# Performance work log

Hardware: AMD Instinct MI355X
Metric: run time of the kernel (lower is better)

The kernel has to match this reference:

```python
import jax, jax.numpy as jnp
import numpy as np

B, C_IN, C_INT, C_OUT, H, W = 4, 1024, 256, 1024, 64, 64
EPS = 1e-5

def conv1x1(x, w, b):
    # x: (B, Cin, H, W), w: (Cout, Cin), b: (Cout,)
    return jnp.einsum('bchw,oc->bohw', x, w) + b[None, :, None, None]

def batchnorm_eval(x, gamma, beta, mean, var):
    inv = gamma / jnp.sqrt(var + EPS)
    return x * inv[None, :, None, None] + (beta - mean * inv)[None, :, None, None]

def setup_inputs() -> dict:
    key = jax.random.key(0)
    ks = jax.random.split(key, 8)
    s_in = 1.0 / np.sqrt(C_IN)
    s_int = 1.0 / np.sqrt(C_INT)
    return {
        'x': jax.random.normal(ks[0], (B, C_IN, H, W), dtype=jnp.float32),
        'w_key': jax.random.normal(ks[1], (C_INT, C_IN), dtype=jnp.float32) * s_in,
        'b_key': jnp.zeros((C_INT,), dtype=jnp.float32),
        'gamma': jnp.ones((C_INT,), dtype=jnp.float32),
        'beta': jnp.zeros((C_INT,), dtype=jnp.float32),
        'mean': jnp.zeros((C_INT,), dtype=jnp.float32),
        'var': jnp.ones((C_INT,), dtype=jnp.float32),
        'w_value': jax.random.normal(ks[2], (C_INT, C_IN), dtype=jnp.float32) * s_in,
        'b_value': jax.random.normal(ks[3], (C_INT,), dtype=jnp.float32) * 0.1,
        'w_out': jax.random.normal(ks[4], (C_OUT, C_INT), dtype=jnp.float32) * s_int,
        'b_out': jax.random.normal(ks[5], (C_OUT,), dtype=jnp.float32) * 0.1,
    }

def reference(x, w_key, b_key, gamma, beta, mean, var, w_value, b_value, w_out, b_out):
    Bb, _, h, w = x.shape
    N = h * w
    # value: 1x1 conv, (B, C, N) -> (B, N, C)
    value = conv1x1(x, w_value, b_value).reshape(Bb, C_INT, N).transpose(0, 2, 1)
    # query/key share the same conv+BN (f_query = f_key)
    qk = batchnorm_eval(conv1x1(x, w_key, b_key), gamma, beta, mean, var).reshape(Bb, C_INT, N)
    query = qk.transpose(0, 2, 1)  # (B, N, C)
    key = qk                        # (B, C, N)
    sim = jnp.einsum('bnc,bcm->bnm', query, key) * (C_INT ** -0.5)  # (B, N, N)
    sim = jax.nn.softmax(sim, axis=-1)
    context = jnp.einsum('bnm,bmc->bnc', sim, value)  # (B, N, C)
    context = context.transpose(0, 2, 1).reshape(Bb, C_INT, h, w)
    return conv1x1(context, w_out, b_out)
```

## Files before the change

kernel.cpp:

```cpp
#include <hip/hip_runtime.h>

#define BATCH 4
#define CIN   1024
#define CI    256
#define CO    1024
#define NSP   4096

typedef __attribute__((ext_vector_type(8))) short bf16x8;
typedef __attribute__((ext_vector_type(4))) float f32x4;
typedef __attribute__((ext_vector_type(2))) unsigned uint2v;

struct __align__(8) us4 { unsigned short x, y, z, w; };

#define DEVI __device__ __forceinline__

DEVI unsigned short f2bf(float f) {
  union { float f; unsigned u; } un; un.f = f;
  unsigned u = un.u;
  u += 0x7FFFu + ((u >> 16) & 1u);
  return (unsigned short)(u >> 16);
}

DEVI unsigned cvtpk(float lo, float hi) {
  unsigned r;
  asm("v_cvt_pk_bf16_f32 %0, %1, %2" : "=v"(r) : "v"(lo), "v"(hi));
  return r;
}

DEVI void gl2lds16(const void* g, void* l) {
  __builtin_amdgcn_global_load_lds(
      (const __attribute__((address_space(1))) void*)g,
      (__attribute__((address_space(3))) void*)l, 16, 0, 0);
}

DEVI f32x4 mfma16(bf16x8 a, bf16x8 b, f32x4 c) {
  return __builtin_amdgcn_mfma_f32_16x16x32_bf16(a, b, c, 0, 0, 0);
}

__global__ __launch_bounds__(256) void k_prep(
    const float* __restrict__ w_key, const float* __restrict__ w_val,
    const float* __restrict__ w_out,
    const float* __restrict__ gamma, const float* __restrict__ beta,
    const float* __restrict__ mean,  const float* __restrict__ var,
    const float* __restrict__ b_key,
    unsigned short* __restrict__ wkv, unsigned short* __restrict__ wob,
    float* __restrict__ sq, float* __restrict__ bq)
{
  int idx = blockIdx.x * 256 + threadIdx.x;
  float wv = (idx < 262144) ? w_key[idx] : w_val[idx - 262144];
  wkv[idx] = f2bf(wv);
  if (idx < 262144) wob[idx] = f2bf(w_out[idx]);
  if (idx < 256) {
    float inv = gamma[idx] * rsqrtf(var[idx] + 1e-5f);
    sq[idx] = 0.25f * inv;
    bq[idx] = 0.25f * (beta[idx] + (b_key[idx] - mean[idx]) * inv);
  }
}

__global__ __launch_bounds__(256) void k_xpose(const float* __restrict__ x,
                                               unsigned short* __restrict__ xT)
{
  __shared__ unsigned short tile[64][65];
  int b = blockIdx.z, k0 = blockIdx.y * 64, n0 = blockIdx.x * 64;
  int tid = threadIdx.x;
  int rr = tid >> 4, cc = tid & 15;
  const float* xb = x + ((size_t)b * CIN + k0) * NSP + n0;
#pragma unroll
  for (int p = 0; p < 4; ++p) {
    int row = p * 16 + rr;
    float4 v = *(const float4*)(xb + (size_t)row * NSP + cc * 4);
    tile[row][cc * 4 + 0] = f2bf(v.x);
    tile[row][cc * 4 + 1] = f2bf(v.y);
    tile[row][cc * 4 + 2] = f2bf(v.z);
    tile[row][cc * 4 + 3] = f2bf(v.w);
  }
  __syncthreads();
  unsigned short* xtb = xT + ((size_t)b * NSP + n0) * CIN + k0;
#pragma unroll
  for (int p = 0; p < 4; ++p) {
    int n = p * 16 + rr;
    int kq = cc * 4;
    us4 pk;
    pk.x = tile[kq + 0][n]; pk.y = tile[kq + 1][n];
    pk.z = tile[kq + 2][n]; pk.w = tile[kq + 3][n];
    *(us4*)(xtb + (size_t)n * CIN + kq) = pk;
  }
}

template<int KDIM>
DEVI void gemm_core(const unsigned short* __restrict__ Ab,
                    const unsigned short* __restrict__ Bb,
                    unsigned short* ldsA, unsigned short* ldsB,
                    f32x4 acc[4][4], int tid)
{
  const int lane = tid & 63, wave = tid >> 6;
  const int q = lane >> 4, ln = lane & 15;
  const int wm = wave & 1, wn = wave >> 1;

  int aoff[4][2], boff[4][2];
#pragma unroll
  for (int f = 0; f < 4; ++f) {
    int ra = wm * 64 + f * 16 + ln;
    aoff[f][0] = (ra * 8 + ((q)     ^ (ra & 7))) * 8;
    aoff[f][1] = (ra * 8 + ((q + 4) ^ (ra & 7))) * 8;
    int rb = wn * 64 + f * 16 + ln;
    boff[f][0] = (rb * 8 + ((q)     ^ (rb & 7))) * 8;
    boff[f][1] = (rb * 8 + ((q + 4) ^ (rb & 7))) * 8;
  }
  int sgo[4];
#pragma unroll
  for (int i = 0; i < 4; ++i) {
    int s = i * 256 + tid;
    int row = s >> 3;
    int c8 = (s & 7) ^ (row & 7);
    sgo[i] = row * KDIM + c8 * 8;
  }
  for (int k0 = 0; k0 < KDIM; k0 += 64) {
#pragma unroll
    for (int i = 0; i < 4; ++i) {
      gl2lds16(Ab + sgo[i] + k0, ldsA + (i * 256 + wave * 64) * 8);
      gl2lds16(Bb + sgo[i] + k0, ldsB + (i * 256 + wave * 64) * 8);
    }
    __syncthreads();
#pragma unroll
    for (int kk = 0; kk < 2; ++kk) {
      bf16x8 af[4], bfr[4];
#pragma unroll
      for (int f = 0; f < 4; ++f) af[f]  = *(const bf16x8*)(ldsA + aoff[f][kk]);
#pragma unroll
      for (int f = 0; f < 4; ++f) bfr[f] = *(const bf16x8*)(ldsB + boff[f][kk]);
#pragma unroll
      for (int mf = 0; mf < 4; ++mf)
#pragma unroll
        for (int nf = 0; nf < 4; ++nf)
          acc[mf][nf] = mfma16(af[mf], bfr[nf], acc[mf][nf]);
    }
    __syncthreads();
  }
}

__global__ __launch_bounds__(256) void k_convqkv(
    const unsigned short* __restrict__ wkv,
    const unsigned short* __restrict__ xT,
    const float* __restrict__ sq, const float* __restrict__ bq,
    const float* __restrict__ bval,
    unsigned short* __restrict__ qkT,
    unsigned short* __restrict__ vv)
{
  __shared__ __align__(16) unsigned short ldsA[128 * 64];
  __shared__ __align__(16) unsigned short ldsB[128 * 64];
  int b = blockIdx.z, m0 = blockIdx.y * 128, n0 = blockIdx.x * 128;
  int tid = threadIdx.x;
  f32x4 z = {0.f, 0.f, 0.f, 0.f};
  f32x4 acc[4][4];
#pragma unroll
  for (int i = 0; i < 4; ++i)
#pragma unroll
    for (int j = 0; j < 4; ++j) acc[i][j] = z;

  gemm_core<CIN>(wkv + (size_t)m0 * CIN, xT + ((size_t)b * NSP + n0) * CIN,
                 ldsA, ldsB, acc, tid);

  int lane = tid & 63, wave = tid >> 6, q = lane >> 4, ln = lane & 15;
  int wm = wave & 1, wn = wave >> 1;
  if (m0 < 256) {
#pragma unroll
    for (int mf = 0; mf < 4; ++mf) {
      int cb = m0 + wm * 64 + mf * 16 + q * 4;
      float s0_ = sq[cb + 0], s1_ = sq[cb + 1], s2_ = sq[cb + 2], s3_ = sq[cb + 3];
      float b0_ = bq[cb + 0], b1_ = bq[cb + 1], b2_ = bq[cb + 2], b3_ = bq[cb + 3];
#pragma unroll
      for (int nf = 0; nf < 4; ++nf) {
        int n = n0 + wn * 64 + nf * 16 + ln;
        us4 pk;
        pk.x = f2bf(acc[mf][nf][0] * s0_ + b0_);
        pk.y = f2bf(acc[mf][nf][1] * s1_ + b1_);
        pk.z = f2bf(acc[mf][nf][2] * s2_ + b2_);
        pk.w = f2bf(acc[mf][nf][3] * s3_ + b3_);
        *(us4*)(qkT + ((size_t)b * NSP + n) * CI + cb) = pk;
      }
    }
  } else {
#pragma unroll
    for (int mf = 0; mf < 4; ++mf) {
      int cb = (m0 - 256) + wm * 64 + mf * 16 + q * 4;
#pragma unroll
      for (int r = 0; r < 4; ++r) {
        float bv = bval[cb + r];
#pragma unroll
        for (int nf = 0; nf < 4; ++nf) {
          int n = n0 + wn * 64 + nf * 16 + ln;
          vv[((size_t)b * CI + (cb + r)) * NSP + n] = f2bf(acc[mf][nf][r] + bv);
        }
      }
    }
  }
}

__global__ __launch_bounds__(256, 2) void k_attn_part(
    const unsigned short* __restrict__ qkT,
    const unsigned short* __restrict__ vv,
    float* __restrict__ Opart,
    float* __restrict__ Lpart)
{
  __shared__ __align__(16) unsigned short Kt[2][32 * 256];
  __shared__ __align__(16) unsigned short Vt[2][256 * 32];
  __shared__ __align__(16) unsigned short Pl[4 * 32 * 40];

  int bid = blockIdx.x;
  int slice = bid & 15, qt = bid >> 4;
  int b = slice >> 2, js = slice & 3;
  int n0 = qt * 128;
  int tid = threadIdx.x, lane = tid & 63, wave = tid >> 6;
  int q = lane >> 4, ln = lane & 15;
  const unsigned short* qkb = qkT + (size_t)b * NSP * CI;
  const unsigned short* vb  = vv  + (size_t)b * CI * NSP;

  bf16x8 Qf0[8], Qf1[8];
  {
    const unsigned short* qr0 = qkb + (size_t)(n0 + wave * 32 + ln) * CI + q * 8;
    const unsigned short* qr1 = qr0 + 16 * CI;
#pragma unroll
    for (int t = 0; t < 8; ++t) Qf0[t] = *(const bf16x8*)(qr0 + t * 32);
#pragma unroll
    for (int t = 0; t < 8; ++t) Qf1[t] = *(const bf16x8*)(qr1 + t * 32);
  }

  int kbA = (ln * 32 + ((q ^ (ln & 7)) & 7)) * 8;
  int kbB = (ln * 32 + (((4 + q) ^ (ln & 7)) & 7)) * 8;
  int vbase = (ln * 4 + ((q ^ ((ln >> 1) & 3)) & 3)) * 8;

  unsigned short* Plw = Pl + wave * (32 * 40);
  int pw0 = ln * 40 + q * 4;
  int pw1 = ln * 40 + 16 + q * 4;
  int pw2 = (ln + 16) * 40 + q * 4;
  int pw3 = (ln + 16) * 40 + 16 + q * 4;
  int pr0 = ln * 40 + q * 8;
  int pr1 = (ln + 16) * 40 + q * 8;

  int gko[4], gvo[4];
#pragma unroll
  for (int i = 0; i < 4; ++i) {
    int s = i * 256 + tid;
    int j = s >> 5, f = s & 31;
    gko[i] = j * CI + ((f & 24) | ((f ^ j) & 7)) * 8;
    int c = s >> 2;
    gvo[i] = c * NSP + ((s ^ (c >> 1)) & 3) * 8;
  }

  f32x4 O0[16], O1[16];
  f32x4 z = {0.f, 0.f, 0.f, 0.f};
#pragma unroll
  for (int cf = 0; cf < 16; ++cf) { O0[cf] = z; O1[cf] = z; }
  float l0c = 0.f, l1c = 0.f;

  int jbase = js * 1024;

#pragma unroll
  for (int i = 0; i < 4; ++i)
    gl2lds16(qkb + (size_t)jbase * CI + gko[i], &Kt[0][(i * 256 + wave * 64) * 8]);
#pragma unroll
  for (int i = 0; i < 4; ++i)
    gl2lds16(vb + jbase + gvo[i], &Vt[0][(i * 256 + wave * 64) * 8]);
  __syncthreads();

  for (int it = 0; it < 32; ++it) {
    int cur = it & 1;

    if (it < 31) {
      int j1 = jbase + (it + 1) * 32;
#pragma unroll
      for (int i = 0; i < 4; ++i)
        gl2lds16(qkb + (size_t)j1 * CI + gko[i],
                 &Kt[cur ^ 1][(i * 256 + wave * 64) * 8]);
#pragma unroll
      for (int i = 0; i < 4; ++i)
        gl2lds16(vb + j1 + gvo[i],
                 &Vt[cur ^ 1][(i * 256 + wave * 64) * 8]);
    }

    const unsigned short* Kc = Kt[cur];
    const unsigned short* Vc = Vt[cur];

    f32x4 s0 = z, s1 = z, s2 = z, s3 = z;
    __builtin_amdgcn_s_setprio(1);
#pragma unroll
    for (int t = 0; t < 8; ++t) {
      int ko = ((t & 1) ? kbB : kbA) + (t >> 1) * 64;
      bf16x8 kf0 = *(const bf16x8*)(Kc + ko);
      bf16x8 kf1 = *(const bf16x8*)(Kc + ko + 4096);
      s0 = mfma16(kf0, Qf0[t], s0);
      s1 = mfma16(kf1, Qf0[t], s1);
      s2 = mfma16(kf0, Qf1[t], s2);
      s3 = mfma16(kf1, Qf1[t], s3);
    }
    __builtin_amdgcn_s_setprio(0);

    float p00 = __expf(s0[0]), p01 = __expf(s0[1]);
    float p02 = __expf(s0[2]), p03 = __expf(s0[3]);
    float p04 = __expf(s1[0]), p05 = __expf(s1[1]);
    float p06 = __expf(s1[2]), p07 = __expf(s1[3]);
    float p10 = __expf(s2[0]), p11 = __expf(s2[1]);
    float p12 = __expf(s2[2]), p13 = __expf(s2[3]);
    float p14 = __expf(s3[0]), p15 = __expf(s3[1]);
    float p16 = __expf(s3[2]), p17 = __expf(s3[3]);

    uint2v w;
    w.x = cvtpk(p00, p01); w.y = cvtpk(p02, p03);
    *(uint2v*)(Plw + pw0) = w;
    w.x = cvtpk(p04, p05); w.y = cvtpk(p06, p07);
    *(uint2v*)(Plw + pw1) = w;
    w.x = cvtpk(p10, p11); w.y = cvtpk(p12, p13);
    *(uint2v*)(Plw + pw2) = w;
    w.x = cvtpk(p14, p15); w.y = cvtpk(p16, p17);
    *(uint2v*)(Plw + pw3) = w;

    l0c += ((p00 + p01) + (p02 + p03)) + ((p04 + p05) + (p06 + p07));
    l1c += ((p10 + p11) + (p12 + p13)) + ((p14 + p15) + (p16 + p17));

    bf16x8 pf0 = *(const bf16x8*)(Plw + pr0);
    bf16x8 pf1 = *(const bf16x8*)(Plw + pr1);
    __builtin_amdgcn_s_setprio(1);
#pragma unroll
    for (int cf = 0; cf < 16; ++cf) {
      bf16x8 vf = *(const bf16x8*)(Vc + vbase + cf * 512);
      O0[cf] = mfma16(pf0, vf, O0[cf]);
      O1[cf] = mfma16(pf1, vf, O1[cf]);
    }
    __builtin_amdgcn_s_setprio(0);

    __syncthreads();
  }

  l0c += __shfl_xor(l0c, 16); l0c += __shfl_xor(l0c, 32);
  l1c += __shfl_xor(l1c, 16); l1c += __shfl_xor(l1c, 32);

  float* Ob = Opart + (size_t)bid * (128 * 256);
  if (lane < 16) {
    Lpart[bid * 128 + wave * 32 + lane] = l0c;
    Lpart[bid * 128 + wave * 32 + 16 + lane] = l1c;
  }
#pragma unroll
  for (int r = 0; r < 4; ++r) {
    int r0 = wave * 32 + q * 4 + r;
#pragma unroll
    for (int cf = 0; cf < 16; ++cf) {
      Ob[r0 * 256 + cf * 16 + ln] = O0[cf][r];
      Ob[(r0 + 16) * 256 + cf * 16 + ln] = O1[cf][r];
    }
  }
}

__global__ __launch_bounds__(256) void k_merge(
    const float* __restrict__ Opart,
    const float* __restrict__ Lpart,
    unsigned short* __restrict__ ctx)
{
  __shared__ float Winv[64];
  int mb = blockIdx.x;
  int b = mb >> 6, qg = mb & 63;
  int qt = qg >> 1, half = qg & 1;
  int ro = half * 64;
  int tid = threadIdx.x;
  int pb0 = qt * 16 + b * 4;

  if (tid < 64) {
    float L = Lpart[(pb0 + 0) * 128 + ro + tid]
            + Lpart[(pb0 + 1) * 128 + ro + tid]
            + Lpart[(pb0 + 2) * 128 + ro + tid]
            + Lpart[(pb0 + 3) * 128 + ro + tid];
    Winv[tid] = 1.0f / L;
  }
  __syncthreads();

  const float* O0 = Opart + ((size_t)(pb0 + 0) * 128 + ro) * 256;
  const float* O1 = Opart + ((size_t)(pb0 + 1) * 128 + ro) * 256;
  const float* O2 = Opart + ((size_t)(pb0 + 2) * 128 + ro) * 256;
  const float* O3 = Opart + ((size_t)(pb0 + 3) * 128 + ro) * 256;
  unsigned short* cb = ctx + ((size_t)b * NSP + qg * 64) * CI;
#pragma unroll 4
  for (int row = 0; row < 64; ++row) {
    float a = (O0[row * 256 + tid] + O1[row * 256 + tid]
             + O2[row * 256 + tid] + O3[row * 256 + tid]) * Winv[row];
    cb[(size_t)row * CI + tid] = f2bf(a);
  }
}

__global__ __launch_bounds__(256) void k_convout(
    const unsigned short* __restrict__ wo,
    const unsigned short* __restrict__ ctx,
    const float* __restrict__ bout,
    float* __restrict__ out)
{
  __shared__ __align__(16) unsigned short ldsA[128 * 64];
  __shared__ __align__(16) unsigned short ldsB[128 * 64];
  int b = blockIdx.z, m0 = blockIdx.y * 128, n0 = blockIdx.x * 128;
  int tid = threadIdx.x;
  f32x4 z = {0.f, 0.f, 0.f, 0.f};
  f32x4 acc[4][4];
#pragma unroll
  for (int i = 0; i < 4; ++i)
#pragma unroll
    for (int j = 0; j < 4; ++j) acc[i][j] = z;

  gemm_core<CI>(wo + (size_t)m0 * CI, ctx + ((size_t)b * NSP + n0) * CI,
                ldsA, ldsB, acc, tid);

  int lane = tid & 63, wave = tid >> 6, q = lane >> 4, ln = lane & 15;
  int wm = wave & 1, wn = wave >> 1;
#pragma unroll
  for (int mf = 0; mf < 4; ++mf) {
    int cb = m0 + wm * 64 + mf * 16 + q * 4;
    float bo0 = bout[cb + 0], bo1 = bout[cb + 1], bo2 = bout[cb + 2], bo3 = bout[cb + 3];
#pragma unroll
    for (int nf = 0; nf < 4; ++nf) {
      int n = n0 + wn * 64 + nf * 16 + ln;
      float* p = out + ((size_t)b * CO + cb) * NSP + n;
      p[0 * (size_t)NSP] = acc[mf][nf][0] + bo0;
      p[1 * (size_t)NSP] = acc[mf][nf][1] + bo1;
      p[2 * (size_t)NSP] = acc[mf][nf][2] + bo2;
      p[3 * (size_t)NSP] = acc[mf][nf][3] + bo3;
    }
  }
}

extern "C" void kernel_launch(void* const* d_in, const int* in_sizes, int n_in,
                              void* d_out, int out_size, void* d_ws, size_t ws_size,
                              hipStream_t stream) {
  const float* x     = (const float*)d_in[0];
  const float* w_key = (const float*)d_in[1];
  const float* b_key = (const float*)d_in[2];
  const float* gamma = (const float*)d_in[3];
  const float* beta  = (const float*)d_in[4];
  const float* mean  = (const float*)d_in[5];
  const float* var   = (const float*)d_in[6];
  const float* w_val = (const float*)d_in[7];
  const float* b_val = (const float*)d_in[8];
  const float* w_out = (const float*)d_in[9];
  const float* b_out = (const float*)d_in[10];
  float* out = (float*)d_out;

  char* ws = (char*)d_ws;
  unsigned short* xT  = (unsigned short*)(ws);
  unsigned short* wkv = (unsigned short*)(ws + 33554432);
  unsigned short* wob = (unsigned short*)(ws + 34603008);
  unsigned short* qkT = (unsigned short*)(ws + 35127296);
  unsigned short* vv  = (unsigned short*)(ws + 43515904);
  unsigned short* ctx = (unsigned short*)(ws + 51904512);
  float* sq = (float*)(ws + 60293120);
  float* bq = (float*)(ws + 60294144);
  float* Opart = (float*)(ws + 60295168);
  float* Lpart = (float*)(ws + 127404032);

  k_prep<<<2048, 256, 0, stream>>>(w_key, w_val, w_out, gamma, beta, mean, var,
                                   b_key, wkv, wob, sq, bq);
  k_xpose<<<dim3(64, 16, 4), 256, 0, stream>>>(x, xT);
  k_convqkv<<<dim3(32, 4, 4), 256, 0, stream>>>(wkv, xT, sq, bq, b_val, qkT, vv);
  k_attn_part<<<512, 256, 0, stream>>>(qkT, vv, Opart, Lpart);
  k_merge<<<256, 256, 0, stream>>>(Opart, Lpart, ctx);
  k_convout<<<dim3(32, 8, 4), 256, 0, stream>>>(wob, ctx, b_out, out);
}
```

Measured before the change: 274.8 us.

## Store attention partials in bf16, double-buffer QKV GEMM, pack transpose writes

The split-attention partial outputs are now packed as bf16 pairs instead of fp32, which halves the Opart write and read traffic between the attention and merge kernels. The merge kernel is rewritten to unpack these pairs and map rows to match. The QKV conv GEMM gets a double-buffered LDS pipeline that prefetches the next K tile while the current one is being computed. The transpose kernel now writes packed 32-bit bf16 pairs with a padded tile. Storing unnormalized partials in bf16 costs some accuracy, and double-buffering doubles LDS use in the conv kernel.

```diff
diff --git a/kernel.cpp b/kernel.cpp
--- a/kernel.cpp
+++ b/kernel.cpp
@@ -60,7 +60,7 @@
 __global__ __launch_bounds__(256) void k_xpose(const float* __restrict__ x,
                                                unsigned short* __restrict__ xT)
 {
-  __shared__ unsigned short tile[64][65];
+  __shared__ unsigned short tile[64][66];
   int b = blockIdx.z, k0 = blockIdx.y * 64, n0 = blockIdx.x * 64;
   int tid = threadIdx.x;
   int rr = tid >> 4, cc = tid & 15;
@@ -69,10 +69,8 @@
   for (int p = 0; p < 4; ++p) {
     int row = p * 16 + rr;
     float4 v = *(const float4*)(xb + (size_t)row * NSP + cc * 4);
-    tile[row][cc * 4 + 0] = f2bf(v.x);
-    tile[row][cc * 4 + 1] = f2bf(v.y);
-    tile[row][cc * 4 + 2] = f2bf(v.z);
-    tile[row][cc * 4 + 3] = f2bf(v.w);
+    *(unsigned*)&tile[row][cc * 4 + 0] = cvtpk(v.x, v.y);
+    *(unsigned*)&tile[row][cc * 4 + 2] = cvtpk(v.z, v.w);
   }
   __syncthreads();
   unsigned short* xtb = xT + ((size_t)b * NSP + n0) * CIN + k0;
@@ -139,6 +137,71 @@
   }
 }
 
+template<int KDIM>
+DEVI void gemm_core_db(const unsigned short* __restrict__ Ab,
+                       const unsigned short* __restrict__ Bb,
+                       unsigned short* ldsA, unsigned short* ldsB,
+                       f32x4 acc[4][4], int tid)
+{
+  const int lane = tid & 63, wave = tid >> 6;
+  const int q = lane >> 4, ln = lane & 15;
+  const int wm = wave & 1, wn = wave >> 1;
+
+  int aoff[4][2], boff[4][2];
+#pragma unroll
+  for (int f = 0; f < 4; ++f) {
+    int ra = wm * 64 + f * 16 + ln;
+    aoff[f][0] = (ra * 8 + ((q)     ^ (ra & 7))) * 8;
+    aoff[f][1] = (ra * 8 + ((q + 4) ^ (ra & 7))) * 8;
+    int rb = wn * 64 + f * 16 + ln;
+    boff[f][0] = (rb * 8 + ((q)     ^ (rb & 7))) * 8;
+    boff[f][1] = (rb * 8 + ((q + 4) ^ (rb & 7))) * 8;
+  }
+  int sgo[4];
+#pragma unroll
+  for (int i = 0; i < 4; ++i) {
+    int s = i * 256 + tid;
+    int row = s >> 3;
+    int c8 = (s & 7) ^ (row & 7);
+    sgo[i] = row * KDIM + c8 * 8;
+  }
+#pragma unroll
+  for (int i = 0; i < 4; ++i) {
+    gl2lds16(Ab + sgo[i], ldsA + (i * 256 + wave * 64) * 8);
+    gl2lds16(Bb + sgo[i], ldsB + (i * 256 + wave * 64) * 8);
+  }
+  __syncthreads();
+
+  for (int k0 = 0; k0 < KDIM; k0 += 64) {
+    const int cur = (k0 >> 6) & 1;
+    unsigned short* A = ldsA + cur * (128 * 64);
+    unsigned short* B = ldsB + cur * (128 * 64);
+    if (k0 + 64 < KDIM) {
+      unsigned short* An = ldsA + (cur ^ 1) * (128 * 64);
+      unsigned short* Bn = ldsB + (cur ^ 1) * (128 * 64);
+#pragma unroll
+      for (int i = 0; i < 4; ++i) {
+        gl2lds16(Ab + sgo[i] + k0 + 64, An + (i * 256 + wave * 64) * 8);
+        gl2lds16(Bb + sgo[i] + k0 + 64, Bn + (i * 256 + wave * 64) * 8);
+      }
+    }
+#pragma unroll
+    for (int kk = 0; kk < 2; ++kk) {
+      bf16x8 af[4], bfr[4];
+#pragma unroll
+      for (int f = 0; f < 4; ++f) af[f]  = *(const bf16x8*)(A + aoff[f][kk]);
+#pragma unroll
+      for (int f = 0; f < 4; ++f) bfr[f] = *(const bf16x8*)(B + boff[f][kk]);
+#pragma unroll
+      for (int mf = 0; mf < 4; ++mf)
+#pragma unroll
+        for (int nf = 0; nf < 4; ++nf)
+          acc[mf][nf] = mfma16(af[mf], bfr[nf], acc[mf][nf]);
+    }
+    __syncthreads();
+  }
+}
+
 __global__ __launch_bounds__(256) void k_convqkv(
     const unsigned short* __restrict__ wkv,
     const unsigned short* __restrict__ xT,
@@ -147,8 +210,8 @@
     unsigned short* __restrict__ qkT,
     unsigned short* __restrict__ vv)
 {
-  __shared__ __align__(16) unsigned short ldsA[128 * 64];
-  __shared__ __align__(16) unsigned short ldsB[128 * 64];
+  __shared__ __align__(16) unsigned short ldsA[2 * 128 * 64];
+  __shared__ __align__(16) unsigned short ldsB[2 * 128 * 64];
   int b = blockIdx.z, m0 = blockIdx.y * 128, n0 = blockIdx.x * 128;
   int tid = threadIdx.x;
   f32x4 z = {0.f, 0.f, 0.f, 0.f};
@@ -158,8 +221,8 @@
 #pragma unroll
     for (int j = 0; j < 4; ++j) acc[i][j] = z;
 
-  gemm_core<CIN>(wkv + (size_t)m0 * CIN, xT + ((size_t)b * NSP + n0) * CIN,
-                 ldsA, ldsB, acc, tid);
+  gemm_core_db<CIN>(wkv + (size_t)m0 * CIN, xT + ((size_t)b * NSP + n0) * CIN,
+                    ldsA, ldsB, acc, tid);
 
   int lane = tid & 63, wave = tid >> 6, q = lane >> 4, ln = lane & 15;
   int wm = wave & 1, wn = wave >> 1;
@@ -200,7 +263,7 @@
 __global__ __launch_bounds__(256, 2) void k_attn_part(
     const unsigned short* __restrict__ qkT,
     const unsigned short* __restrict__ vv,
-    float* __restrict__ Opart,
+    unsigned* __restrict__ Opart,
     float* __restrict__ Lpart)
 {
   __shared__ __align__(16) unsigned short Kt[2][32 * 256];
@@ -335,24 +398,22 @@
   l0c += __shfl_xor(l0c, 16); l0c += __shfl_xor(l0c, 32);
   l1c += __shfl_xor(l1c, 16); l1c += __shfl_xor(l1c, 32);
 
-  float* Ob = Opart + (size_t)bid * (128 * 256);
+  unsigned* Ob = Opart + (size_t)bid * (64 * 256);
   if (lane < 16) {
     Lpart[bid * 128 + wave * 32 + lane] = l0c;
     Lpart[bid * 128 + wave * 32 + 16 + lane] = l1c;
   }
 #pragma unroll
   for (int r = 0; r < 4; ++r) {
-    int r0 = wave * 32 + q * 4 + r;
-#pragma unroll
-    for (int cf = 0; cf < 16; ++cf) {
-      Ob[r0 * 256 + cf * 16 + ln] = O0[cf][r];
-      Ob[(r0 + 16) * 256 + cf * 16 + ln] = O1[cf][r];
-    }
+    int rp = wave * 16 + q * 4 + r;
+#pragma unroll
+    for (int cf = 0; cf < 16; ++cf)
+      Ob[rp * 256 + cf * 16 + ln] = cvtpk(O0[cf][r], O1[cf][r]);
   }
 }
 
 __global__ __launch_bounds__(256) void k_merge(
-    const float* __restrict__ Opart,
+    const unsigned* __restrict__ Opart,
     const float* __restrict__ Lpart,
     unsigned short* __restrict__ ctx)
 {
@@ -360,29 +421,36 @@
   int mb = blockIdx.x;
   int b = mb >> 6, qg = mb & 63;
   int qt = qg >> 1, half = qg & 1;
-  int ro = half * 64;
   int tid = threadIdx.x;
   int pb0 = qt * 16 + b * 4;
 
   if (tid < 64) {
-    float L = Lpart[(pb0 + 0) * 128 + ro + tid]
-            + Lpart[(pb0 + 1) * 128 + ro + tid]
-            + Lpart[(pb0 + 2) * 128 + ro + tid]
-            + Lpart[(pb0 + 3) * 128 + ro + tid];
+    int row = half * 64 + tid;
+    float L = Lpart[(pb0 + 0) * 128 + row]
+            + Lpart[(pb0 + 1) * 128 + row]
+            + Lpart[(pb0 + 2) * 128 + row]
+            + Lpart[(pb0 + 3) * 128 + row];
     Winv[tid] = 1.0f / L;
   }
   __syncthreads();
 
-  const float* O0 = Opart + ((size_t)(pb0 + 0) * 128 + ro) * 256;
-  const float* O1 = Opart + ((size_t)(pb0 + 1) * 128 + ro) * 256;
-  const float* O2 = Opart + ((size_t)(pb0 + 2) * 128 + ro) * 256;
-  const float* O3 = Opart + ((size_t)(pb0 + 3) * 128 + ro) * 256;
+  const unsigned* P0 = Opart + ((size_t)(pb0 + 0) * 64 + half * 32) * 256;
+  const unsigned* P1 = Opart + ((size_t)(pb0 + 1) * 64 + half * 32) * 256;
+  const unsigned* P2 = Opart + ((size_t)(pb0 + 2) * 64 + half * 32) * 256;
+  const unsigned* P3 = Opart + ((size_t)(pb0 + 3) * 64 + half * 32) * 256;
   unsigned short* cb = ctx + ((size_t)b * NSP + qg * 64) * CI;
 #pragma unroll 4
-  for (int row = 0; row < 64; ++row) {
-    float a = (O0[row * 256 + tid] + O1[row * 256 + tid]
-             + O2[row * 256 + tid] + O3[row * 256 + tid]) * Winv[row];
-    cb[(size_t)row * CI + tid] = f2bf(a);
+  for (int rp = 0; rp < 32; ++rp) {
+    unsigned u0 = P0[rp * 256 + tid], u1 = P1[rp * 256 + tid];
+    unsigned u2 = P2[rp * 256 + tid], u3 = P3[rp * 256 + tid];
+    float lo = __uint_as_float(u0 << 16) + __uint_as_float(u1 << 16)
+             + __uint_as_float(u2 << 16) + __uint_as_float(u3 << 16);
+    float hi = __uint_as_float(u0 & 0xFFFF0000u) + __uint_as_float(u1 & 0xFFFF0000u)
+             + __uint_as_float(u2 & 0xFFFF0000u) + __uint_as_float(u3 & 0xFFFF0000u);
+    int ra = (rp & 15) + ((rp >> 4) << 5);
+    int rb = ra + 16;
+    cb[(size_t)ra * CI + tid] = f2bf(lo * Winv[ra]);
+    cb[(size_t)rb * CI + tid] = f2bf(hi * Winv[rb]);
   }
 }
 
@@ -449,7 +517,7 @@
   unsigned short* ctx = (unsigned short*)(ws + 51904512);
   float* sq = (float*)(ws + 60293120);
   float* bq = (float*)(ws + 60294144);
-  float* Opart = (float*)(ws + 60295168);
+  unsigned* Opart = (unsigned*)(ws + 60295168);
   float* Lpart = (float*)(ws + 127404032);
 
   k_prep<<<2048, 256, 0, stream>>>(w_key, w_val, w_out, gamma, beta, mean, var,
```

Measured after the change: 262.2 us. 1.05x faster.
